# Optimization experiments

Measured on AMD Instinct MI355X. Metric: run time of the kernel, lower is better.

## Reference

```python
import jax, jax.numpy as jnp
import numpy as np

D_EMBED, D_K, D_V = 1024, 64, 64
B, S = 4, 4096


def setup_inputs() -> dict:
    key = jax.random.key(0)
    k1, k2, k3, k4 = jax.random.split(key, 4)
    x = jax.random.normal(k1, (B, S, D_EMBED), dtype=jnp.float32)
    # nn.Linear(d_embed, d) stores weight as [d, d_embed]
    Wq = jax.random.normal(k2, (D_K, D_EMBED), dtype=jnp.float32) * (D_EMBED ** -0.5)
    Wk = jax.random.normal(k3, (D_K, D_EMBED), dtype=jnp.float32) * (D_EMBED ** -0.5)
    Wv = jax.random.normal(k4, (D_V, D_EMBED), dtype=jnp.float32) * (D_EMBED ** -0.5)
    return {"x": x, "Wq": Wq, "Wk": Wk, "Wv": Wv}


def reference(x, Wq, Wk, Wv):
    # self-attention: y = z = x
    key = jnp.einsum('bse,ke->bsk', x, Wk)
    query = jnp.einsum('bse,ke->bsk', x, Wq)
    value = jnp.einsum('bse,ve->bsv', x, Wv)
    d_k = key.shape[-1]
    weight = jnp.einsum('bqk,bsk->bqs', query, key) / (d_k ** 0.5)
    # Faithful to torch: tril then masked_fill(weight == 0, -inf)
    weight = jnp.tril(weight)
    weight = jnp.where(weight == 0, -jnp.inf, weight)
    weight = jax.nn.softmax(weight, axis=-1)
    return jnp.einsum('bqs,bsv->bqv', weight, value)
```

## Files before the change

### kernel.cpp

```cpp
#include <hip/hip_runtime.h>
#include <hip/hip_bf16.h>


typedef short s16x8 __attribute__((ext_vector_type(8)));
typedef float f32x4 __attribute__((ext_vector_type(4)));
typedef float f32x16 __attribute__((ext_vector_type(16)));
typedef unsigned u32x2 __attribute__((ext_vector_type(2)));
typedef union { unsigned u[4]; s16x8 v; } pfrag;

#define MFMA16(a, b, c) __builtin_amdgcn_mfma_f32_16x16x32_bf16(a, b, c, 0, 0, 0)
#define MFMA32(a, b, c) __builtin_amdgcn_mfma_f32_32x32x16_bf16(a, b, c, 0, 0, 0)

constexpr int SEQ = 4096;
constexpr int DE  = 1024;

__device__ __forceinline__ short f2bf(float f) {
    union { float f; unsigned u; } v; v.f = f;
    unsigned r = (v.u + 0x7FFFu + ((v.u >> 16) & 1u)) >> 16;
    return (short)r;
}
__device__ __forceinline__ unsigned fbits(float f) { union { float f; unsigned u; } v; v.f = f; return v.u; }
__device__ __forceinline__ float bitsf(unsigned u) { union { unsigned u; float f; } v; v.u = u; return v.f; }
__device__ __forceinline__ unsigned pk2(float a, float b) {
    return (fbits(b) & 0xFFFF0000u) | (fbits(a) >> 16);
}

#define GLDS(gp, lp)                                                          \
    __builtin_amdgcn_global_load_lds(                                         \
        (const __attribute__((address_space(1))) unsigned int*)(gp),          \
        (__attribute__((address_space(3))) unsigned int*)(lp), 16, 0, 0)

__global__ __launch_bounds__(256) void k_convw(const float* __restrict__ Wq,
                                               const float* __restrict__ Wk,
                                               const float* __restrict__ Wv,
                                               short* __restrict__ Wb) {
    int i = (blockIdx.x * 256 + threadIdx.x) * 4;
    if (i >= 192 * 1024) return;
    int n = i >> 10, k = i & 1023;
    const float* src; float sc;
    if (n < 64)       { src = Wq + n * 1024;         sc = 0.18033688011112042f; }
    else if (n < 128) { src = Wk + (n - 64) * 1024;  sc = 1.0f; }
    else              { src = Wv + (n - 128) * 1024; sc = 1.0f; }
    float4 v = *(const float4*)(src + k);
    short4 o;
    o.x = f2bf(v.x * sc); o.y = f2bf(v.y * sc);
    o.z = f2bf(v.z * sc); o.w = f2bf(v.w * sc);
    *(short4*)(Wb + i) = o;
}

__global__ __launch_bounds__(512) void k_proj(const float* __restrict__ x,
                                              const short* __restrict__ Wb,
                                              short* __restrict__ Qs,
                                              short* __restrict__ Ks,
                                              short* __restrict__ Vt) {
    __shared__ __align__(16) char lds[2][40960];
    const int tid  = threadIdx.x;
    const int lane = tid & 63;
    const int c = lane & 15, g = (lane >> 4) & 3;
    const int wv = tid >> 6;
    const int rg = wv & 3, nh = wv >> 2;
    const int n0 = nh * 96;
    const int m0 = blockIdx.x * 64;

    const int Ar  = tid >> 4;
    const int Acs = ((tid & 15) << 4) ^ ((Ar & 7) << 4);
    const char* aS0 = (const char*)x + (((size_t)(m0 + Ar)) << 12) + Acs;
    const char* aS1 = aS0 + ((size_t)32 << 12);
    const int Wr  = tid >> 3;
    const int Wcs = ((tid & 7) << 4) ^ ((Wr & 7) << 4);
    const char* wS0 = (const char*)Wb + (((size_t)Wr) << 11) + Wcs;
    const char* wS1 = wS0 + ((size_t)64 << 11);
    const char* wS2 = wS0 + ((size_t)128 << 11);

    char* db0 = &lds[0][0] + tid * 16;
    char* db1 = &lds[1][0] + tid * 16;

    const int arow = rg * 16 + c;
    const int swz  = (c & 7) << 4;
    const char* aR[2] = { &lds[0][0] + arow * 256, &lds[1][0] + arow * 256 };
    const char* wR[2][6];
#pragma unroll
    for (int nf = 0; nf < 6; nf++) {
        int wrow = n0 + nf * 16 + c;
        wR[0][nf] = &lds[0][0] + 16384 + wrow * 128;
        wR[1][nf] = &lds[1][0] + 16384 + wrow * 128;
    }

    f32x4 acc[6];
#pragma unroll
    for (int i = 0; i < 6; i++) acc[i] = (f32x4){0.f, 0.f, 0.f, 0.f};

#define PSTAGE(kk, db) {                                  \
        GLDS(aS0 + (kk) * 256, (db));                     \
        GLDS(aS1 + (kk) * 256, (db) + 8192);              \
        GLDS(wS0 + (kk) * 128, (db) + 16384);             \
        GLDS(wS1 + (kk) * 128, (db) + 24576);             \
        GLDS(wS2 + (kk) * 128, (db) + 32768); }

#define PCOMPUTE(bi) {                                                         \
        _Pragma("unroll")                                                      \
        for (int kc = 0; kc < 2; kc++) {                                       \
            float4 a0 = *(const float4*)(aR[bi] + ((kc*128 + g*32)      ^ swz)); \
            float4 a1 = *(const float4*)(aR[bi] + ((kc*128 + g*32 + 16) ^ swz)); \
            s16x8 a;                                                           \
            a[0]=f2bf(a0.x); a[1]=f2bf(a0.y); a[2]=f2bf(a0.z); a[3]=f2bf(a0.w); \
            a[4]=f2bf(a1.x); a[5]=f2bf(a1.y); a[6]=f2bf(a1.z); a[7]=f2bf(a1.w); \
            _Pragma("unroll")                                                  \
            for (int nf = 0; nf < 6; nf++) {                                   \
                s16x8 bfr = *(const s16x8*)(wR[bi][nf] + ((kc*64 + g*16) ^ swz)); \
                acc[nf] = MFMA16(a, bfr, acc[nf]);                             \
            }                                                                  \
        } }

    PSTAGE(0, db0);
    PSTAGE(1, db1);

    for (int kk = 0; kk < 15; kk++) {
        asm volatile("s_waitcnt vmcnt(5)" ::: "memory");
        __builtin_amdgcn_sched_barrier(0);
        __builtin_amdgcn_s_barrier();
        if (kk & 1) PCOMPUTE(1) else PCOMPUTE(0)
        asm volatile("s_waitcnt lgkmcnt(0)" ::: "memory");
        __builtin_amdgcn_sched_barrier(0);
        __builtin_amdgcn_s_barrier();
        if (kk < 14) { if (kk & 1) PSTAGE(kk + 2, db1) else PSTAGE(kk + 2, db0) }
    }
    asm volatile("s_waitcnt vmcnt(0)" ::: "memory");
    __builtin_amdgcn_sched_barrier(0);
    __builtin_amdgcn_s_barrier();
    PCOMPUTE(1)
#undef PSTAGE
#undef PCOMPUTE

#pragma unroll
    for (int nf = 0; nf < 6; nf++) {
        int col16 = n0 + nf * 16;
        if (col16 < 64) {
            int col = col16 + c;
#pragma unroll
            for (int r = 0; r < 4; r++)
                Qs[(size_t)(m0 + rg * 16 + g * 4 + r) * 64 + col] = f2bf(acc[nf][r]);
        } else if (col16 < 128) {
            int col = col16 - 64 + c;
#pragma unroll
            for (int r = 0; r < 4; r++)
                Ks[(size_t)(m0 + rg * 16 + g * 4 + r) * 64 + col] = f2bf(acc[nf][r]);
        } else {
            int d  = col16 - 128 + c;
            int mm = m0 + rg * 16 + g * 4;
            int bt = mm >> 12, s0 = mm & (SEQ - 1);
            short4 o;
            o.x = f2bf(acc[nf][0]); o.y = f2bf(acc[nf][1]);
            o.z = f2bf(acc[nf][2]); o.w = f2bf(acc[nf][3]);
            *(short4*)(Vt + ((size_t)(bt * 64 + d)) * SEQ + s0) = o;
        }
    }
}

#define PACKPH(sa, sb, u0, u1, u2, u3) {                                       \
    unsigned A0 = pk2(sa[0], sa[1]),   B0 = pk2(sa[2], sa[3]);                 \
    unsigned A1 = pk2(sa[4], sa[5]),   B1 = pk2(sa[6], sa[7]);                 \
    unsigned A2 = pk2(sa[8], sa[9]),   B2 = pk2(sa[10], sa[11]);               \
    unsigned A3 = pk2(sa[12], sa[13]), B3 = pk2(sa[14], sa[15]);               \
    u32x2 r0_ = __builtin_amdgcn_permlane32_swap(A0, A1, false, false);        \
    u32x2 r1_ = __builtin_amdgcn_permlane32_swap(B0, B1, false, false);        \
    u32x2 r2_ = __builtin_amdgcn_permlane32_swap(A2, A3, false, false);        \
    u32x2 r3_ = __builtin_amdgcn_permlane32_swap(B2, B3, false, false);        \
    u0.u[0] = r0_[0]; u0.u[1] = r1_[0]; u0.u[2] = r0_[1]; u0.u[3] = r1_[1];    \
    u1.u[0] = r2_[0]; u1.u[1] = r3_[0]; u1.u[2] = r2_[1]; u1.u[3] = r3_[1];    \
    A0 = pk2(sb[0], sb[1]);   B0 = pk2(sb[2], sb[3]);                          \
    A1 = pk2(sb[4], sb[5]);   B1 = pk2(sb[6], sb[7]);                          \
    A2 = pk2(sb[8], sb[9]);   B2 = pk2(sb[10], sb[11]);                        \
    A3 = pk2(sb[12], sb[13]); B3 = pk2(sb[14], sb[15]);                        \
    r0_ = __builtin_amdgcn_permlane32_swap(A0, A1, false, false);              \
    r1_ = __builtin_amdgcn_permlane32_swap(B0, B1, false, false);              \
    r2_ = __builtin_amdgcn_permlane32_swap(A2, A3, false, false);              \
    r3_ = __builtin_amdgcn_permlane32_swap(B2, B3, false, false);              \
    u2.u[0] = r0_[0]; u2.u[1] = r1_[0]; u2.u[2] = r0_[1]; u2.u[3] = r1_[1];    \
    u3.u[0] = r2_[0]; u3.u[1] = r3_[0]; u3.u[2] = r2_[1]; u3.u[3] = r3_[1]; }

__global__ __launch_bounds__(256, 2) void k_attn(const short* __restrict__ Qs,
                                                 const short* __restrict__ Ks,
                                                 const short* __restrict__ Vt,
                                                 float* __restrict__ pws) {
    __shared__ __align__(16) char smem[2][16384];

    int tid = threadIdx.x;
    int l = tid & 63, wv = tid >> 6;
    int q = l & 31, hi = l >> 5;

    int ub = blockIdx.x >> 2, bt = blockIdx.x & 3;
    int u = ub, j = 31, cs = 8;
    while (u >= cs) { u -= cs; --j; cs = (j + 4) >> 2; }
    int seg = u;
    int kb0 = seg << 9;
    int kend_t = min(j * 128 + 128, kb0 + 512);
    const int R = (kend_t - kb0 + 63) >> 6;
    const int q0 = j * 128 + wv * 32;
    const int mycend = q0 + 32;

    const short* Qb = Qs + (size_t)bt * SEQ * 64;
    const short* Kb = Ks + (size_t)bt * SEQ * 64;
    const short* Vb = Vt + (size_t)bt * 64 * SEQ;

    s16x8 qf[4];
#pragma unroll
    for (int d = 0; d < 4; d++)
        qf[d] = *(const s16x8*)(Qb + (size_t)(q0 + q) * 64 + d * 16 + hi * 8);

    const int g0r = (tid * 2) >> 3,     g0c = (tid * 2) & 7;
    const int g1r = (tid * 2 + 1) >> 3, g1c = (tid * 2 + 1) & 7;
    const int kofs0 = g0r * 128 + ((g0c ^ (g0r & 7)) << 4);
    const int kofs1 = g1r * 128 + ((g1c ^ (g1r & 7)) << 4);

    s16x8 kreg0, kreg1, vreg0, vreg1;
#define LOADREGS(kb) {                                                         \
        kreg0 = *(const s16x8*)(Kb + (size_t)((kb) + g0r) * 64 + g0c * 8);     \
        kreg1 = *(const s16x8*)(Kb + (size_t)((kb) + g1r) * 64 + g1c * 8);     \
        vreg0 = *(const s16x8*)(Vb + (size_t)g0r * SEQ + (kb) + g0c * 8);      \
        vreg1 = *(const s16x8*)(Vb + (size_t)g1r * SEQ + (kb) + g1c * 8); }
#define WRITELDS(b) {                                                          \
        *(s16x8*)(&smem[b][0] + kofs0) = kreg0;                                \
        *(s16x8*)(&smem[b][0] + kofs1) = kreg1;                                \
        *(s16x8*)(&smem[b][0] + 8192 + kofs0) = vreg0;                         \
        *(s16x8*)(&smem[b][0] + 8192 + kofs1) = vreg1; }

    f32x16 o0 = {}, o1 = {};
    float m = -1e30f, ll = 0.f;
    const int qs7 = q & 7;

    LOADREGS(kb0);
    WRITELDS(0);
    if (R > 1) LOADREGS(kb0 + 64);
    asm volatile("s_waitcnt lgkmcnt(0)" ::: "memory");
    __builtin_amdgcn_sched_barrier(0);
    __builtin_amdgcn_s_barrier();

    for (int r = 0; r < R; r++) {
        if (r + 1 < R) WRITELDS((r + 1) & 1);
        if (r + 2 < R) LOADREGS(kb0 + (r + 2) * 64);

        const char* kl = &smem[r & 1][0];
        const char* vl = kl + 8192;
        s16x8 kf[8], vf[8];
#pragma unroll
        for (int dd = 0; dd < 4; dd++) {
            int ch = ((2 * dd + hi) ^ qs7) << 4;
            kf[dd]     = *(const s16x8*)(kl + q * 128 + ch);
            kf[4 + dd] = *(const s16x8*)(kl + (32 + q) * 128 + ch);
            vf[dd]     = *(const s16x8*)(vl + q * 128 + ch);
            vf[4 + dd] = *(const s16x8*)(vl + (32 + q) * 128 + ch);
        }
        asm volatile("s_waitcnt lgkmcnt(0)" ::: "memory");
        __builtin_amdgcn_sched_barrier(0);

        int k0 = kb0 + r * 64;
        if (k0 < mycend) {
            f32x16 sa = {}, sb = {};
            __builtin_amdgcn_s_setprio(1);
#pragma unroll
            for (int dd = 0; dd < 4; dd++) {
                sa = MFMA32(kf[dd],     qf[dd], sa);
                sb = MFMA32(kf[4 + dd], qf[dd], sb);
            }
            __builtin_amdgcn_s_setprio(0);
            if (k0 + 31 > q0) {
#pragma unroll
                for (int rr = 0; rr < 16; rr++) {
                    int kv = k0 + (rr & 3) + 8 * (rr >> 2) + 4 * hi;
                    if (kv > q0 + q) sa[rr] = -3.0e38f;
                }
            }
            if (k0 + 63 > q0) {
#pragma unroll
                for (int rr = 0; rr < 16; rr++) {
                    int kv = k0 + 32 + (rr & 3) + 8 * (rr >> 2) + 4 * hi;
                    if (kv > q0 + q) sb[rr] = -3.0e38f;
                }
            }
            float t0 = -3.0e38f, t1 = -3.0e38f;
#pragma unroll
            for (int rr = 0; rr < 16; rr++) { t0 = fmaxf(t0, sa[rr]); t1 = fmaxf(t1, sb[rr]); }
            float tm = fmaxf(t0, t1);
            u32x2 sw = __builtin_amdgcn_permlane32_swap(fbits(tm), fbits(tm), false, false);
            tm = fmaxf(bitsf(sw[0]), bitsf(sw[1]));
            if (__any(tm > m + 8.0f)) {
                float mn = fmaxf(m, tm);
                float sc_ = __builtin_amdgcn_exp2f(m - mn);
                m = mn;
                ll *= sc_;
                o0 *= sc_; o1 *= sc_;
            }
            float ss = 0.f;
#pragma unroll
            for (int rr = 0; rr < 16; rr++) {
                sa[rr] = __builtin_amdgcn_exp2f(sa[rr] - m);
                sb[rr] = __builtin_amdgcn_exp2f(sb[rr] - m);
                ss += sa[rr] + sb[rr];
            }
            sw = __builtin_amdgcn_permlane32_swap(fbits(ss), fbits(ss), false, false);
            ss = bitsf(sw[0]) + bitsf(sw[1]);
            ll += ss;

            pfrag u0_, u1_, u2_, u3_;
            PACKPH(sa, sb, u0_, u1_, u2_, u3_);
            __builtin_amdgcn_s_setprio(1);
            o0 = MFMA32(vf[0], u0_.v, o0);
            o0 = MFMA32(vf[1], u1_.v, o0);
            o0 = MFMA32(vf[2], u2_.v, o0);
            o0 = MFMA32(vf[3], u3_.v, o0);
            o1 = MFMA32(vf[4], u0_.v, o1);
            o1 = MFMA32(vf[5], u1_.v, o1);
            o1 = MFMA32(vf[6], u2_.v, o1);
            o1 = MFMA32(vf[7], u3_.v, o1);
            __builtin_amdgcn_s_setprio(0);
        }

        __builtin_amdgcn_s_barrier();
    }
#undef LOADREGS
#undef WRITELDS

    float* p = pws + ((((size_t)(bt * 32 + j) * 4 + wv) * 8 + seg)) * 2112;
#pragma unroll
    for (int rr = 0; rr < 16; rr++) {
        int dv = (rr & 3) + 8 * (rr >> 2) + 4 * hi;
        p[dv * 32 + q]        = o0[rr];
        p[(dv + 32) * 32 + q] = o1[rr];
    }
    if (hi == 0) { p[2048 + q] = m; p[2080 + q] = ll; }
}

__global__ __launch_bounds__(256) void k_comb(const float* __restrict__ pws,
                                              float* __restrict__ out) {
    int b = blockIdx.x;
    int w = b & 3, j = (b >> 2) & 31, bt = b >> 7;
    int nseg = (j + 4) >> 2;

    int tid = threadIdx.x;
    int q = tid >> 3, dv0 = (tid & 7) * 8;
    const float* base = pws + ((size_t)(bt * 32 + j) * 4 + w) * 8 * 2112;

    float ms[8], wsg[8];
    float M = -1e30f;
#pragma unroll
    for (int s = 0; s < 8; s++) {
        if (s < nseg) { ms[s] = base[s * 2112 + 2048 + q]; M = fmaxf(M, ms[s]); }
    }
    float L = 0.f;
#pragma unroll
    for (int s = 0; s < 8; s++) {
        if (s < nseg) {
            wsg[s] = __builtin_amdgcn_exp2f(ms[s] - M);
            L += wsg[s] * base[s * 2112 + 2080 + q];
        }
    }
    float inv = 1.0f / L;
    float res[8];
#pragma unroll
    for (int i = 0; i < 8; i++) res[i] = 0.f;
#pragma unroll
    for (int s = 0; s < 8; s++) {
        if (s < nseg) {
            const float* po = base + s * 2112;
#pragma unroll
            for (int i = 0; i < 8; i++) res[i] += wsg[s] * po[(dv0 + i) * 32 + q];
        }
    }
    float* op = out + ((size_t)bt * SEQ + j * 128 + w * 32 + q) * 64 + dv0;
    float4 f0 = {res[0] * inv, res[1] * inv, res[2] * inv, res[3] * inv};
    float4 f1 = {res[4] * inv, res[5] * inv, res[6] * inv, res[7] * inv};
    *(float4*)op = f0;
    *(float4*)(op + 4) = f1;
}

extern "C" void kernel_launch(void* const* d_in, const int* in_sizes, int n_in,
                              void* d_out, int out_size, void* d_ws, size_t ws_size,
                              hipStream_t stream) {
    const float* x  = (const float*)d_in[0];
    const float* Wq = (const float*)d_in[1];
    const float* Wk = (const float*)d_in[2];
    const float* Wv = (const float*)d_in[3];
    float* out = (float*)d_out;

    char* ws = (char*)d_ws;
    short* Wb = (short*)ws;
    short* Qs = (short*)(ws + 393216);
    short* Ks = (short*)(ws + 393216 + 2097152);
    short* Vt = (short*)(ws + 393216 + 2 * 2097152);
    float* pP = (float*)(ws + 6684672);

    k_convw<<<dim3(192), dim3(256), 0, stream>>>(Wq, Wk, Wv, Wb);
    k_proj <<<dim3(256), dim3(512), 0, stream>>>(x, Wb, Qs, Ks, Vt);
    k_attn <<<dim3(576), dim3(256), 0, stream>>>(Qs, Ks, Vt, pP);
    k_comb <<<dim3(512), dim3(256), 0, stream>>>(pP, out);
}
```

Baseline: 72.23 us.

## Halve proj and attention tile sizes, use async global-to-LDS loads in attention

The projection kernel now uses 32-row tiles with 48-column slices per wave, which doubles its grid and lowers LDS per block so four blocks can share a CU. The attention kernel splits the KV range into 256-key segments instead of 512, giving more blocks, and the combine kernel is extended to merge up to 16 segments. Attention K/V staging switches from register loads followed by LDS writes to direct global-to-LDS copies with a vmcnt-based double buffer. The aim is to fill more CUs and cut register staging, at the cost of more partial results to write and merge and more W reloads per row tile.

Result: slower. 73.89 us (+2.3%).

```diff
diff --git a/kernel.cpp b/kernel.cpp
--- a/kernel.cpp
+++ b/kernel.cpp
@@ -48,24 +48,23 @@
     *(short4*)(Wb + i) = o;
 }
 
-__global__ __launch_bounds__(512) void k_proj(const float* __restrict__ x,
-                                              const short* __restrict__ Wb,
-                                              short* __restrict__ Qs,
-                                              short* __restrict__ Ks,
-                                              short* __restrict__ Vt) {
-    __shared__ __align__(16) char lds[2][40960];
+__global__ __launch_bounds__(512, 4) void k_proj(const float* __restrict__ x,
+                                                 const short* __restrict__ Wb,
+                                                 short* __restrict__ Qs,
+                                                 short* __restrict__ Ks,
+                                                 short* __restrict__ Vt) {
+    __shared__ __align__(16) char lds[2][32768];
     const int tid  = threadIdx.x;
     const int lane = tid & 63;
     const int c = lane & 15, g = (lane >> 4) & 3;
     const int wv = tid >> 6;
-    const int rg = wv & 3, nh = wv >> 2;
-    const int n0 = nh * 96;
-    const int m0 = blockIdx.x * 64;
+    const int rg = wv & 1, nh = wv >> 1;
+    const int n0 = nh * 48;
+    const int m0 = blockIdx.x * 32;
 
     const int Ar  = tid >> 4;
     const int Acs = ((tid & 15) << 4) ^ ((Ar & 7) << 4);
     const char* aS0 = (const char*)x + (((size_t)(m0 + Ar)) << 12) + Acs;
-    const char* aS1 = aS0 + ((size_t)32 << 12);
     const int Wr  = tid >> 3;
     const int Wcs = ((tid & 7) << 4) ^ ((Wr & 7) << 4);
     const char* wS0 = (const char*)Wb + (((size_t)Wr) << 11) + Wcs;
@@ -78,24 +77,23 @@
     const int arow = rg * 16 + c;
     const int swz  = (c & 7) << 4;
     const char* aR[2] = { &lds[0][0] + arow * 256, &lds[1][0] + arow * 256 };
-    const char* wR[2][6];
-#pragma unroll
-    for (int nf = 0; nf < 6; nf++) {
+    const char* wR[2][3];
+#pragma unroll
+    for (int nf = 0; nf < 3; nf++) {
         int wrow = n0 + nf * 16 + c;
-        wR[0][nf] = &lds[0][0] + 16384 + wrow * 128;
-        wR[1][nf] = &lds[1][0] + 16384 + wrow * 128;
-    }
-
-    f32x4 acc[6];
-#pragma unroll
-    for (int i = 0; i < 6; i++) acc[i] = (f32x4){0.f, 0.f, 0.f, 0.f};
+        wR[0][nf] = &lds[0][0] + 8192 + wrow * 128;
+        wR[1][nf] = &lds[1][0] + 8192 + wrow * 128;
+    }
+
+    f32x4 acc[3];
+#pragma unroll
+    for (int i = 0; i < 3; i++) acc[i] = (f32x4){0.f, 0.f, 0.f, 0.f};
 
 #define PSTAGE(kk, db) {                                  \
         GLDS(aS0 + (kk) * 256, (db));                     \
-        GLDS(aS1 + (kk) * 256, (db) + 8192);              \
-        GLDS(wS0 + (kk) * 128, (db) + 16384);             \
-        GLDS(wS1 + (kk) * 128, (db) + 24576);             \
-        GLDS(wS2 + (kk) * 128, (db) + 32768); }
+        GLDS(wS0 + (kk) * 128, (db) + 8192);              \
+        GLDS(wS1 + (kk) * 128, (db) + 16384);             \
+        GLDS(wS2 + (kk) * 128, (db) + 24576); }
 
 #define PCOMPUTE(bi) {                                                         \
         _Pragma("unroll")                                                      \
@@ -106,7 +104,7 @@
             a[0]=f2bf(a0.x); a[1]=f2bf(a0.y); a[2]=f2bf(a0.z); a[3]=f2bf(a0.w); \
             a[4]=f2bf(a1.x); a[5]=f2bf(a1.y); a[6]=f2bf(a1.z); a[7]=f2bf(a1.w); \
             _Pragma("unroll")                                                  \
-            for (int nf = 0; nf < 6; nf++) {                                   \
+            for (int nf = 0; nf < 3; nf++) {                                   \
                 s16x8 bfr = *(const s16x8*)(wR[bi][nf] + ((kc*64 + g*16) ^ swz)); \
                 acc[nf] = MFMA16(a, bfr, acc[nf]);                             \
             }                                                                  \
@@ -116,7 +114,7 @@
     PSTAGE(1, db1);
 
     for (int kk = 0; kk < 15; kk++) {
-        asm volatile("s_waitcnt vmcnt(5)" ::: "memory");
+        asm volatile("s_waitcnt vmcnt(4)" ::: "memory");
         __builtin_amdgcn_sched_barrier(0);
         __builtin_amdgcn_s_barrier();
         if (kk & 1) PCOMPUTE(1) else PCOMPUTE(0)
@@ -133,7 +131,7 @@
 #undef PCOMPUTE
 
 #pragma unroll
-    for (int nf = 0; nf < 6; nf++) {
+    for (int nf = 0; nf < 3; nf++) {
         int col16 = n0 + nf * 16;
         if (col16 < 64) {
             int col = col16 + c;
@@ -190,11 +188,11 @@
     int q = l & 31, hi = l >> 5;
 
     int ub = blockIdx.x >> 2, bt = blockIdx.x & 3;
-    int u = ub, j = 31, cs = 8;
-    while (u >= cs) { u -= cs; --j; cs = (j + 4) >> 2; }
+    int u = ub, j = 31, cs = 16;
+    while (u >= cs) { u -= cs; --j; cs = (j + 2) >> 1; }
     int seg = u;
-    int kb0 = seg << 9;
-    int kend_t = min(j * 128 + 128, kb0 + 512);
+    int kb0 = seg << 8;
+    int kend_t = min(j * 128 + 128, kb0 + 256);
     const int R = (kend_t - kb0 + 63) >> 6;
     const int q0 = j * 128 + wv * 32;
     const int mycend = q0 + 32;
@@ -208,37 +206,29 @@
     for (int d = 0; d < 4; d++)
         qf[d] = *(const s16x8*)(Qb + (size_t)(q0 + q) * 64 + d * 16 + hi * 8);
 
-    const int g0r = (tid * 2) >> 3,     g0c = (tid * 2) & 7;
-    const int g1r = (tid * 2 + 1) >> 3, g1c = (tid * 2 + 1) & 7;
-    const int kofs0 = g0r * 128 + ((g0c ^ (g0r & 7)) << 4);
-    const int kofs1 = g1r * 128 + ((g1c ^ (g1r & 7)) << 4);
-
-    s16x8 kreg0, kreg1, vreg0, vreg1;
-#define LOADREGS(kb) {                                                         \
-        kreg0 = *(const s16x8*)(Kb + (size_t)((kb) + g0r) * 64 + g0c * 8);     \
-        kreg1 = *(const s16x8*)(Kb + (size_t)((kb) + g1r) * 64 + g1c * 8);     \
-        vreg0 = *(const s16x8*)(Vb + (size_t)g0r * SEQ + (kb) + g0c * 8);      \
-        vreg1 = *(const s16x8*)(Vb + (size_t)g1r * SEQ + (kb) + g1c * 8); }
-#define WRITELDS(b) {                                                          \
-        *(s16x8*)(&smem[b][0] + kofs0) = kreg0;                                \
-        *(s16x8*)(&smem[b][0] + kofs1) = kreg1;                                \
-        *(s16x8*)(&smem[b][0] + 8192 + kofs0) = vreg0;                         \
-        *(s16x8*)(&smem[b][0] + 8192 + kofs1) = vreg1; }
+    const int row8 = l >> 3;
+    const int scs  = (l & 7) ^ row8;
+
+#define ASTAGE(kb, b) {                                                        \
+        _Pragma("unroll")                                                      \
+        for (int i = 0; i < 2; i++) {                                          \
+            GLDS(Kb + (((size_t)((kb) + wv*16 + i*8 + row8)) << 6) + scs*8,    \
+                 &smem[b][0] + (wv*16 + i*8)*128);                             \
+            GLDS(Vb + (size_t)(wv*16 + i*8 + row8) * SEQ + (kb) + scs*8,       \
+                 &smem[b][0] + 8192 + (wv*16 + i*8)*128); } }
 
     f32x16 o0 = {}, o1 = {};
     float m = -1e30f, ll = 0.f;
     const int qs7 = q & 7;
 
-    LOADREGS(kb0);
-    WRITELDS(0);
-    if (R > 1) LOADREGS(kb0 + 64);
-    asm volatile("s_waitcnt lgkmcnt(0)" ::: "memory");
-    __builtin_amdgcn_sched_barrier(0);
-    __builtin_amdgcn_s_barrier();
+    ASTAGE(kb0, 0);
+    if (R > 1) ASTAGE(kb0 + 64, 1);
 
     for (int r = 0; r < R; r++) {
-        if (r + 1 < R) WRITELDS((r + 1) & 1);
-        if (r + 2 < R) LOADREGS(kb0 + (r + 2) * 64);
+        if (r == R - 1) asm volatile("s_waitcnt vmcnt(0)" ::: "memory");
+        else            asm volatile("s_waitcnt vmcnt(4)" ::: "memory");
+        __builtin_amdgcn_sched_barrier(0);
+        __builtin_amdgcn_s_barrier();
 
         const char* kl = &smem[r & 1][0];
         const char* vl = kl + 8192;
@@ -251,8 +241,6 @@
             vf[dd]     = *(const s16x8*)(vl + q * 128 + ch);
             vf[4 + dd] = *(const s16x8*)(vl + (32 + q) * 128 + ch);
         }
-        asm volatile("s_waitcnt lgkmcnt(0)" ::: "memory");
-        __builtin_amdgcn_sched_barrier(0);
 
         int k0 = kb0 + r * 64;
         if (k0 < mycend) {
@@ -316,12 +304,14 @@
             __builtin_amdgcn_s_setprio(0);
         }
 
+        asm volatile("s_waitcnt lgkmcnt(0)" ::: "memory");
+        __builtin_amdgcn_sched_barrier(0);
         __builtin_amdgcn_s_barrier();
-    }
-#undef LOADREGS
-#undef WRITELDS
-
-    float* p = pws + ((((size_t)(bt * 32 + j) * 4 + wv) * 8 + seg)) * 2112;
+        if (r + 2 < R) { if (r & 1) ASTAGE(kb0 + (r + 2) * 64, 1) else ASTAGE(kb0 + (r + 2) * 64, 0) }
+    }
+#undef ASTAGE
+
+    float* p = pws + ((((size_t)(bt * 32 + j) * 4 + wv) * 16 + seg)) * 2112;
 #pragma unroll
     for (int rr = 0; rr < 16; rr++) {
         int dv = (rr & 3) + 8 * (rr >> 2) + 4 * hi;
@@ -335,21 +325,21 @@
                                               float* __restrict__ out) {
     int b = blockIdx.x;
     int w = b & 3, j = (b >> 2) & 31, bt = b >> 7;
-    int nseg = (j + 4) >> 2;
+    int nseg = (j + 2) >> 1;
 
     int tid = threadIdx.x;
     int q = tid >> 3, dv0 = (tid & 7) * 8;
-    const float* base = pws + ((size_t)(bt * 32 + j) * 4 + w) * 8 * 2112;
-
-    float ms[8], wsg[8];
+    const float* base = pws + ((size_t)(bt * 32 + j) * 4 + w) * 16 * 2112;
+
+    float ms[16], wsg[16];
     float M = -1e30f;
 #pragma unroll
-    for (int s = 0; s < 8; s++) {
+    for (int s = 0; s < 16; s++) {
         if (s < nseg) { ms[s] = base[s * 2112 + 2048 + q]; M = fmaxf(M, ms[s]); }
     }
     float L = 0.f;
 #pragma unroll
-    for (int s = 0; s < 8; s++) {
+    for (int s = 0; s < 16; s++) {
         if (s < nseg) {
             wsg[s] = __builtin_amdgcn_exp2f(ms[s] - M);
             L += wsg[s] * base[s * 2112 + 2080 + q];
@@ -360,7 +350,7 @@
 #pragma unroll
     for (int i = 0; i < 8; i++) res[i] = 0.f;
 #pragma unroll
-    for (int s = 0; s < 8; s++) {
+    for (int s = 0; s < 16; s++) {
         if (s < nseg) {
             const float* po = base + s * 2112;
 #pragma unroll
@@ -390,8 +380,8 @@
     short* Vt = (short*)(ws + 393216 + 2 * 2097152);
     float* pP = (float*)(ws + 6684672);
 
-    k_convw<<<dim3(192), dim3(256), 0, stream>>>(Wq, Wk, Wv, Wb);
-    k_proj <<<dim3(256), dim3(512), 0, stream>>>(x, Wb, Qs, Ks, Vt);
-    k_attn <<<dim3(576), dim3(256), 0, stream>>>(Qs, Ks, Vt, pP);
-    k_comb <<<dim3(512), dim3(256), 0, stream>>>(pP, out);
-}
+    k_convw<<<dim3(192),  dim3(256), 0, stream>>>(Wq, Wk, Wv, Wb);
+    k_proj <<<dim3(512),  dim3(512), 0, stream>>>(x, Wb, Qs, Ks, Vt);
+    k_attn <<<dim3(1088), dim3(256), 0, stream>>>(Qs, Ks, Vt, pP);
+    k_comb <<<dim3(512),  dim3(256), 0, stream>>>(pP, out);
+}
```
